# Performance work log

Measured on AMD Instinct MI355X. Metric: run time of the kernel, lower is better.

Reference implementation:

```python
import jax, jax.numpy as jnp
import numpy as np

B, S = 256, 32          # sequence layout for the final (b, s, 1) reshape
BATCH = B * S           # 8192 flattened rows processed per call
IN, U, OUT = 32, 128, 1 # sensory inputs, interneurons, motor outputs
UNFOLDS = 6             # semi-implicit ODE solver unfolds


def _syn_sigmoid(v, mu, sigma):
    # v: [B, P]; mu, sigma: [P, Q] -> [B, P, Q] per-synapse gate
    return jax.nn.sigmoid(sigma * (v[:, :, None] - mu))


def setup_inputs() -> dict:
    key = jax.random.key(0)
    ks = jax.random.split(key, 12)
    inputs = jax.random.normal(ks[0], (BATCH, IN), dtype=jnp.float32)
    state = jax.random.normal(ks[1], (BATCH, U), dtype=jnp.float32)
    # adjacency in {-1, 0, 1} (wiring polarity), baked into W / erev as in _get_variables
    sens_adj = jax.random.randint(ks[2], (IN, U), -1, 2).astype(jnp.float32)
    adj = jax.random.randint(ks[3], (U, U), -1, 2).astype(jnp.float32)
    sensory_mu = jax.random.uniform(ks[4], (IN, U)) * 0.5 + 0.3
    sensory_sigma = jax.random.uniform(ks[5], (IN, U)) * 5.0 + 3.0
    # NOTE: original applies +w_init_min OUTSIDE the |adj| mask; reproduced faithfully
    sensory_W = jnp.abs(sens_adj) * jax.random.uniform(ks[6], (IN, U)) * 0.9 + 0.1
    sensory_erev = sens_adj  # erev_init_factor = 1
    mu = jax.random.uniform(ks[7], (U, U)) * 0.5 + 0.3
    sigma = jax.random.uniform(ks[8], (U, U)) * 5.0 + 3.0
    W = jnp.abs(adj) * jax.random.uniform(ks[9], (U, U)) * 0.9 + 0.1
    erev = adj
    vleak = jax.random.uniform(ks[10], (U,)) * 0.4 - 0.2
    gleak = jnp.ones((U,), jnp.float32)        # gleak_init_min == gleak_init_max == 1
    cm_t = jnp.ones((U,), jnp.float32) * 0.5    # cm_init_min == cm_init_max == 0.5
    in_w = jnp.ones((IN,), jnp.float32)         # affine input mapping (init ones/zeros)
    in_b = jnp.zeros((IN,), jnp.float32)
    out_w = jnp.ones((OUT,), jnp.float32)       # affine output mapping
    out_b = jnp.zeros((OUT,), jnp.float32)
    return dict(inputs=inputs, state=state, sensory_mu=sensory_mu,
                sensory_sigma=sensory_sigma, sensory_W=sensory_W,
                sensory_erev=sensory_erev, mu=mu, sigma=sigma, W=W, erev=erev,
                vleak=vleak, gleak=gleak, cm_t=cm_t, in_w=in_w, in_b=in_b,
                out_w=out_w, out_b=out_b, b=B, s=S)


def reference(inputs, state, sensory_mu, sensory_sigma, sensory_W, sensory_erev,
              mu, sigma, W, erev, vleak, gleak, cm_t, in_w, in_b, out_w, out_b,
              b, s):
    x = inputs * in_w + in_b                                   # _map_inputs (Affine)
    # sensory synapse activations, computed once: [BATCH, IN, U]
    sa = sensory_W * _syn_sigmoid(x, sensory_mu, sensory_sigma)
    w_num_s = jnp.sum(sa * sensory_erev, axis=1)               # [BATCH, U]
    w_den_s = jnp.sum(sa, axis=1)                              # [BATCH, U]

    def step(v, _):
        wa = W * _syn_sigmoid(v, mu, sigma)                    # [BATCH, U, U]
        w_num = jnp.sum(wa * erev, axis=1) + w_num_s
        w_den = jnp.sum(wa, axis=1) + w_den_s
        v_new = (cm_t * v + gleak * vleak + w_num) / (cm_t + gleak + w_den)
        return v_new, None

    v, _ = jax.lax.scan(step, state, None, length=UNFOLDS)
    outputs = (v[:, :OUT] * out_w + out_b).reshape(b, s, 1)    # _map_outputs
    return outputs, v
```

## Files before the change

kernel.cpp:

```cpp
#include <hip/hip_runtime.h>

#define NIN 32
#define NU  128
#define RPB 4
#define NQ  4
#define UNFOLDS 6
#define LOG2E 1.44269504088896340736f
#define TBL_N 4096
#define TBL_SCALE 128.0f
#define TBL_OFF 2048.5f

typedef float float4v __attribute__((ext_vector_type(4)));

#define SPN (NIN * NU)
#define RPN (NU * NU)

__device__ __constant__ int RLOC[5] = {0, 18, 36, 82, 128};
__device__ __constant__ int SLOC[5] = {0, 4, 8, 20, 32};

__global__ void pack_params(const float* __restrict__ mu,
                            const float* __restrict__ sig,
                            const float* __restrict__ W,
                            const float* __restrict__ erev,
                            float4v* __restrict__ out_e,
                            float4v* __restrict__ out_t, int n) {
    int idx = blockIdx.x * blockDim.x + threadIdx.x;
    if (idx < n) {
        float sg = sig[idx];
        float s2 = -LOG2E * sg;
        float sm2 = -s2 * mu[idx];
        float Wv = W[idx];
        float We = Wv * erev[idx];
        out_e[idx] = (float4v){s2, sm2, We, Wv};
        out_t[idx] = (float4v){TBL_SCALE * s2,
                               __builtin_fmaf(TBL_SCALE, sm2, TBL_OFF), We, Wv};
    }
}

#define EVAL_PAIR(p, v0, v1, n0, d0, n1, d1)                                   \
    {                                                                          \
        float e0 = __builtin_amdgcn_exp2f(__builtin_fmaf((p).x, (v0), (p).y)); \
        float e1 = __builtin_amdgcn_exp2f(__builtin_fmaf((p).x, (v1), (p).y)); \
        float a1 = 1.0f + e1;                                                  \
        float P  = __builtin_fmaf(e0, a1, a1);                                 \
        float rq = __builtin_amdgcn_rcpf(P);                                   \
        float s0 = rq * a1;                                                    \
        float s1 = __builtin_fmaf(rq, e0, rq);                                 \
        (n0) = __builtin_fmaf((p).z, s0, (n0));                                \
        (d0) = __builtin_fmaf((p).w, s0, (d0));                                \
        (n1) = __builtin_fmaf((p).z, s1, (n1));                                \
        (d1) = __builtin_fmaf((p).w, s1, (d1));                                \
    }

#define EVAL_TBL(p, v, n_, d_)                                                 \
    {                                                                          \
        float af = __builtin_fmaf((p).x, (v), (p).y);                          \
        af = __builtin_amdgcn_fmed3f(af, 0.0f, (float)(TBL_N - 1));            \
        float s = tbl[(unsigned)af];                                           \
        (n_) = __builtin_fmaf((p).z, s, (n_));                                 \
        (d_) = __builtin_fmaf((p).w, s, (d_));                                 \
    }

__global__ __launch_bounds__(512, 8)
void wormnet_main(const float* __restrict__ inputs,
                  const float* __restrict__ state,
                  const float4v* __restrict__ spe, const float4v* __restrict__ spt,
                  const float4v* __restrict__ rpe, const float4v* __restrict__ rpt,
                  const float* __restrict__ vleak,
                  const float* __restrict__ gleak,
                  const float* __restrict__ cm_t,
                  const float* __restrict__ in_w, const float* __restrict__ in_b,
                  const float* __restrict__ out_w, const float* __restrict__ out_b,
                  float* __restrict__ out_y,
                  float* __restrict__ out_v)
{
    __shared__ __align__(16) float tbl[TBL_N];
    __shared__ __align__(16) float xs[NIN * RPB];
    __shared__ __align__(16) float vs[NU * RPB];
    __shared__ float rn[RPB][NQ][NU];
    __shared__ float rd[RPB][NQ][NU];

    const int tid  = threadIdx.x;
    const int j    = tid & (NU - 1);
    const int q    = tid >> 7;
    const int base = blockIdx.x * RPB;

    #pragma unroll
    for (int k = tid; k < TBL_N; k += 512) {
        float t = (float)(k - TBL_N / 2) * (1.0f / TBL_SCALE);
        tbl[k] = __builtin_amdgcn_rcpf(1.0f + __builtin_amdgcn_exp2f(t));
    }

    if (tid < NIN * RPB) {
        int i = tid & (NIN - 1);
        int r = tid >> 5;
        xs[i * RPB + r] = inputs[(base + r) * NIN + i] * in_w[i] + in_b[i];
    }
    float vold = state[(base + q) * NU + j];
    vs[j * RPB + q] = vold;
    __syncthreads();

    const int slo = SLOC[q], shi = SLOC[q + 1];
    const int rlo = RLOC[q], rhi = RLOC[q + 1];

    float numS[RPB], denS[RPB];
    #pragma unroll
    for (int r = 0; r < RPB; ++r) { numS[r] = 0.0f; denS[r] = 0.0f; }
    if (q < 2) {
        const float4v* pp = spe + slo * NU + j;
        #pragma unroll 2
        for (int i = slo; i < shi; ++i) {
            float4v p = pp[0]; pp += NU;
            float4v xv = *(const float4v*)&xs[i * RPB];
            EVAL_PAIR(p, xv[0], xv[1], numS[0], denS[0], numS[1], denS[1]);
            EVAL_PAIR(p, xv[2], xv[3], numS[2], denS[2], numS[3], denS[3]);
        }
    } else {
        const float4v* pp = spt + slo * NU + j;
        #pragma unroll 2
        for (int i = slo; i < shi; ++i) {
            float4v p = pp[0]; pp += NU;
            float4v xv = *(const float4v*)&xs[i * RPB];
            #pragma unroll
            for (int r = 0; r < RPB; ++r) { EVAL_TBL(p, xv[r], numS[r], denS[r]); }
        }
    }

    const float cm = cm_t[j];
    const float gl = gleak[j];
    const float glvl = gl * vleak[j];
    const float cg = cm + gl;

    for (int u = 0; u < UNFOLDS; ++u) {
        float num[RPB], den[RPB];
        #pragma unroll
        for (int r = 0; r < RPB; ++r) { num[r] = numS[r]; den[r] = denS[r]; }

        if (q < 2) {
            const float4v* pp = rpe + rlo * NU + j;
            #pragma unroll 2
            for (int i = rlo; i < rhi; ++i) {
                float4v p = pp[0]; pp += NU;
                float4v vv = *(const float4v*)&vs[i * RPB];
                EVAL_PAIR(p, vv[0], vv[1], num[0], den[0], num[1], den[1]);
                EVAL_PAIR(p, vv[2], vv[3], num[2], den[2], num[3], den[3]);
            }
        } else {
            const float4v* pp = rpt + rlo * NU + j;
            #pragma unroll 2
            for (int i = rlo; i < rhi; ++i) {
                float4v p = pp[0]; pp += NU;
                float4v vv = *(const float4v*)&vs[i * RPB];
                #pragma unroll
                for (int r = 0; r < RPB; ++r) { EVAL_TBL(p, vv[r], num[r], den[r]); }
            }
        }

        #pragma unroll
        for (int r = 0; r < RPB; ++r) {
            rn[r][q][j] = num[r];
            rd[r][q][j] = den[r];
        }
        __syncthreads();

        {
            float tn = (rn[q][0][j] + rn[q][1][j]) + (rn[q][2][j] + rn[q][3][j]);
            float td = (rd[q][0][j] + rd[q][1][j]) + (rd[q][2][j] + rd[q][3][j]);
            float vn = (__builtin_fmaf(cm, vold, glvl) + tn)
                       * __builtin_amdgcn_rcpf(cg + td);
            vold = vn;
            vs[j * RPB + q] = vn;
        }
        __syncthreads();
    }

    out_v[(base + q) * NU + j] = vold;
    if (j == 0) {
        out_y[base + q] = __builtin_fmaf(vold, out_w[0], out_b[0]);
    }
}

extern "C" void kernel_launch(void* const* d_in, const int* in_sizes, int n_in,
                              void* d_out, int out_size, void* d_ws, size_t ws_size,
                              hipStream_t stream) {
    const float* inputs  = (const float*)d_in[0];
    const float* state   = (const float*)d_in[1];
    const float* smu     = (const float*)d_in[2];
    const float* ssig    = (const float*)d_in[3];
    const float* sW      = (const float*)d_in[4];
    const float* serev   = (const float*)d_in[5];
    const float* rmu     = (const float*)d_in[6];
    const float* rsig    = (const float*)d_in[7];
    const float* rW      = (const float*)d_in[8];
    const float* rerev   = (const float*)d_in[9];
    const float* vleak   = (const float*)d_in[10];
    const float* gleak   = (const float*)d_in[11];
    const float* cm_t    = (const float*)d_in[12];
    const float* in_w    = (const float*)d_in[13];
    const float* in_b    = (const float*)d_in[14];
    const float* out_w   = (const float*)d_in[15];
    const float* out_b   = (const float*)d_in[16];

    const int batch = in_sizes[1] / NU;
    float* out_y = (float*)d_out;
    float* out_v = (float*)d_out + batch;

    float4v* spe = (float4v*)d_ws;
    float4v* spt = spe + SPN;
    float4v* rpe = spt + SPN;
    float4v* rpt = rpe + RPN;

    hipLaunchKernelGGL(pack_params, dim3((SPN + 255) / 256), dim3(256), 0, stream,
                       smu, ssig, sW, serev, spe, spt, SPN);
    hipLaunchKernelGGL(pack_params, dim3((RPN + 255) / 256), dim3(256), 0, stream,
                       rmu, rsig, rW, rerev, rpe, rpt, RPN);

    dim3 grid(batch / RPB), block(NU * NQ);
    hipLaunchKernelGGL(wormnet_main, grid, block, 0, stream,
                       inputs, state, spe, spt, rpe, rpt,
                       vleak, gleak, cm_t, in_w, in_b, out_w, out_b,
                       out_y, out_v);
}
```

Measured before the change: 266.5 us.

## Process eight rows per block with fp16-packed partial sums and rebalanced splits

Doubles the rows handled per block from four to eight, so each packed synapse parameter load serves twice as many batch rows. Each thread now owns two rows in the final reduction. The cross-quarter partial numerator and denominator are packed into one fp16 pair per slot to keep shared memory in budget. The split points between the exact and table-lookup sigmoid paths are rebalanced for the larger per-row workload. In exchange, register pressure rises, the grid has half as many blocks, and the fp16 partial sums add rounding error to the ODE update.

```diff
diff --git a/kernel.cpp b/kernel.cpp
--- a/kernel.cpp
+++ b/kernel.cpp
@@ -2,7 +2,7 @@
 
 #define NIN 32
 #define NU  128
-#define RPB 4
+#define RPB 8
 #define NQ  4
 #define UNFOLDS 6
 #define LOG2E 1.44269504088896340736f
@@ -11,12 +11,13 @@
 #define TBL_OFF 2048.5f
 
 typedef float float4v __attribute__((ext_vector_type(4)));
+typedef __fp16 half2v __attribute__((ext_vector_type(2)));
 
 #define SPN (NIN * NU)
 #define RPN (NU * NU)
 
-__device__ __constant__ int RLOC[5] = {0, 18, 36, 82, 128};
-__device__ __constant__ int SLOC[5] = {0, 4, 8, 20, 32};
+__device__ __constant__ int RLOC[5] = {0, 27, 54, 91, 128};
+__device__ __constant__ int SLOC[5] = {0, 7, 14, 23, 32};
 
 __global__ void pack_params(const float* __restrict__ mu,
                             const float* __restrict__ sig,
@@ -77,12 +78,12 @@
     __shared__ __align__(16) float tbl[TBL_N];
     __shared__ __align__(16) float xs[NIN * RPB];
     __shared__ __align__(16) float vs[NU * RPB];
-    __shared__ float rn[RPB][NQ][NU];
-    __shared__ float rd[RPB][NQ][NU];
+    __shared__ unsigned prt[RPB][NQ][NU];
 
     const int tid  = threadIdx.x;
     const int j    = tid & (NU - 1);
     const int q    = tid >> 7;
+    const int u0   = q * 2;
     const int base = blockIdx.x * RPB;
 
     #pragma unroll
@@ -96,8 +97,12 @@
         int r = tid >> 5;
         xs[i * RPB + r] = inputs[(base + r) * NIN + i] * in_w[i] + in_b[i];
     }
-    float vold = state[(base + q) * NU + j];
-    vs[j * RPB + q] = vold;
+    float vold[2];
+    #pragma unroll
+    for (int k = 0; k < 2; ++k) {
+        vold[k] = state[(base + u0 + k) * NU + j];
+        vs[j * RPB + u0 + k] = vold[k];
+    }
     __syncthreads();
 
     const int slo = SLOC[q], shi = SLOC[q + 1];
@@ -108,21 +113,25 @@
     for (int r = 0; r < RPB; ++r) { numS[r] = 0.0f; denS[r] = 0.0f; }
     if (q < 2) {
         const float4v* pp = spe + slo * NU + j;
-        #pragma unroll 2
         for (int i = slo; i < shi; ++i) {
             float4v p = pp[0]; pp += NU;
-            float4v xv = *(const float4v*)&xs[i * RPB];
-            EVAL_PAIR(p, xv[0], xv[1], numS[0], denS[0], numS[1], denS[1]);
-            EVAL_PAIR(p, xv[2], xv[3], numS[2], denS[2], numS[3], denS[3]);
+            float4v xa = *(const float4v*)&xs[i * RPB];
+            float4v xb = *(const float4v*)&xs[i * RPB + 4];
+            EVAL_PAIR(p, xa[0], xa[1], numS[0], denS[0], numS[1], denS[1]);
+            EVAL_PAIR(p, xa[2], xa[3], numS[2], denS[2], numS[3], denS[3]);
+            EVAL_PAIR(p, xb[0], xb[1], numS[4], denS[4], numS[5], denS[5]);
+            EVAL_PAIR(p, xb[2], xb[3], numS[6], denS[6], numS[7], denS[7]);
         }
     } else {
         const float4v* pp = spt + slo * NU + j;
-        #pragma unroll 2
         for (int i = slo; i < shi; ++i) {
             float4v p = pp[0]; pp += NU;
-            float4v xv = *(const float4v*)&xs[i * RPB];
+            float4v xa = *(const float4v*)&xs[i * RPB];
+            float4v xb = *(const float4v*)&xs[i * RPB + 4];
             #pragma unroll
-            for (int r = 0; r < RPB; ++r) { EVAL_TBL(p, xv[r], numS[r], denS[r]); }
+            for (int r = 0; r < 4; ++r) { EVAL_TBL(p, xa[r], numS[r], denS[r]); }
+            #pragma unroll
+            for (int r = 0; r < 4; ++r) { EVAL_TBL(p, xb[r], numS[r + 4], denS[r + 4]); }
         }
     }
 
@@ -138,45 +147,63 @@
 
         if (q < 2) {
             const float4v* pp = rpe + rlo * NU + j;
-            #pragma unroll 2
             for (int i = rlo; i < rhi; ++i) {
                 float4v p = pp[0]; pp += NU;
-                float4v vv = *(const float4v*)&vs[i * RPB];
-                EVAL_PAIR(p, vv[0], vv[1], num[0], den[0], num[1], den[1]);
-                EVAL_PAIR(p, vv[2], vv[3], num[2], den[2], num[3], den[3]);
+                float4v va = *(const float4v*)&vs[i * RPB];
+                float4v vb = *(const float4v*)&vs[i * RPB + 4];
+                EVAL_PAIR(p, va[0], va[1], num[0], den[0], num[1], den[1]);
+                EVAL_PAIR(p, va[2], va[3], num[2], den[2], num[3], den[3]);
+                EVAL_PAIR(p, vb[0], vb[1], num[4], den[4], num[5], den[5]);
+                EVAL_PAIR(p, vb[2], vb[3], num[6], den[6], num[7], den[7]);
             }
         } else {
             const float4v* pp = rpt + rlo * NU + j;
-            #pragma unroll 2
             for (int i = rlo; i < rhi; ++i) {
                 float4v p = pp[0]; pp += NU;
-                float4v vv = *(const float4v*)&vs[i * RPB];
+                float4v va = *(const float4v*)&vs[i * RPB];
+                float4v vb = *(const float4v*)&vs[i * RPB + 4];
                 #pragma unroll
-                for (int r = 0; r < RPB; ++r) { EVAL_TBL(p, vv[r], num[r], den[r]); }
+                for (int r = 0; r < 4; ++r) { EVAL_TBL(p, va[r], num[r], den[r]); }
+                #pragma unroll
+                for (int r = 0; r < 4; ++r) { EVAL_TBL(p, vb[r], num[r + 4], den[r + 4]); }
             }
         }
 
         #pragma unroll
         for (int r = 0; r < RPB; ++r) {
-            rn[r][q][j] = num[r];
-            rd[r][q][j] = den[r];
+            half2v pk = __builtin_amdgcn_cvt_pkrtz(num[r], den[r]);
+            prt[r][q][j] = __builtin_bit_cast(unsigned, pk);
         }
         __syncthreads();
 
-        {
-            float tn = (rn[q][0][j] + rn[q][1][j]) + (rn[q][2][j] + rn[q][3][j]);
-            float td = (rd[q][0][j] + rd[q][1][j]) + (rd[q][2][j] + rd[q][3][j]);
-            float vn = (__builtin_fmaf(cm, vold, glvl) + tn)
+        #pragma unroll
+        for (int k = 0; k < 2; ++k) {
+            const int r = u0 + k;
+            float tn = 0.0f, td = 0.0f;
+            #pragma unroll
+            for (int qq = 0; qq < NQ; ++qq) {
+                half2v h = __builtin_bit_cast(half2v, prt[r][qq][j]);
+                tn += (float)h[0];
+                td += (float)h[1];
+            }
+            float vn = (__builtin_fmaf(cm, vold[k], glvl) + tn)
                        * __builtin_amdgcn_rcpf(cg + td);
-            vold = vn;
-            vs[j * RPB + q] = vn;
+            vold[k] = vn;
+            vs[j * RPB + r] = vn;
         }
         __syncthreads();
     }
 
-    out_v[(base + q) * NU + j] = vold;
+    #pragma unroll
+    for (int k = 0; k < 2; ++k) {
+        out_v[(base + u0 + k) * NU + j] = vold[k];
+    }
     if (j == 0) {
-        out_y[base + q] = __builtin_fmaf(vold, out_w[0], out_b[0]);
+        const float ow = out_w[0], ob = out_b[0];
+        #pragma unroll
+        for (int k = 0; k < 2; ++k) {
+            out_y[base + u0 + k] = __builtin_fmaf(vold[k], ow, ob);
+        }
     }
 }
 
```

Measured after the change: 259.9 us. 1.03x faster.
